# Kernel tuning notes

Measured on AMD Instinct MI355X. Metric: run time of the kernel, lower is better.

## Reference

```python
import jax, jax.numpy as jnp
import numpy as np

N = 50000          # total nodes
B = 10             # graphs in batch
NPG = N // B       # nodes per graph (equal-sized graphs)
E = 800000         # edges
IN_DIM = 128
HID = 128
NHEAD = 4
DHEAD = HID // NHEAD
T = 1000
SLOPE = 0.2        # leaky_relu negative slope
ALPHA_L = 2.0


def _ln(x, g=None, b=None, eps=1e-5):
    mu = jnp.mean(x, axis=-1, keepdims=True)
    var = jnp.var(x, axis=-1, keepdims=True)
    y = (x - mu) * jax.lax.rsqrt(var + eps)
    if g is not None:
        y = y * g + b
    return y


def _gatv2(h, src, dst, Ws, Wd, a, b):
    # DGL GATv2Conv, share_weights=False, residual=False, bias=True, activation=gelu
    fs = (h @ Ws).reshape(N, NHEAD, DHEAD)
    fd = (h @ Wd).reshape(N, NHEAD, DHEAD)
    # per-edge attention logits [E, NHEAD]
    e = jnp.sum(jax.nn.leaky_relu(fs[src] + fd[dst], SLOPE) * a, axis=-1)
    # edge softmax grouped by destination node
    m = jax.ops.segment_max(e, dst, num_segments=N)
    ee = jnp.exp(e - m[dst])
    den = jax.ops.segment_sum(ee, dst, num_segments=N)
    alpha = ee / den[dst]                                  # [E, NHEAD]
    rst = jax.ops.segment_sum(alpha[..., None] * fs[src], dst, num_segments=N)
    rst = jax.nn.gelu(rst + b.reshape(1, NHEAD, DHEAD), approximate=False)
    return rst.reshape(N, HID)


def _forward(x, noise, sab, somab, time_emb,
             Ws0, Wd0, a0, b0, g0, be0,
             Ws1, Wd1, a1, b1, g1, be1,
             Wo1, bo1, Wo2, bo2, src, dst, t):
    # sample_q: statistics-matched signed noise
    miu = jnp.mean(x, axis=0)
    std = jnp.std(x, axis=0, ddof=1)          # torch.std is unbiased
    nz = _ln(noise) * std + miu
    nz = jnp.sign(x) * jnp.abs(nz)
    s1 = jnp.repeat(sab[t], NPG)[:, None]
    s2 = jnp.repeat(somab[t], NPG)[:, None]
    x_t = s1 * x + s2 * nz
    temb = jnp.repeat(time_emb[t], NPG, axis=0)
    # Denoising_Unet
    h = jnp.concatenate([x_t, temb], axis=1)   # [N, IN_DIM+HID]
    h = _ln(_gatv2(h, src, dst, Ws0, Wd0, a0, b0), g0, be0)
    h_in = h
    h = _gatv2(h, src, dst, Ws1, Wd1, a1, b1)
    h = _ln(h + h_in, g1, be1)                 # residual (shapes match)
    out = jax.nn.relu(h @ Wo1 + bo1) @ Wo2 + bo2
    # loss_fn
    mse = jnp.mean((out - x) ** 2)
    on = out / jnp.maximum(jnp.linalg.norm(out, axis=-1, keepdims=True), 1e-12)
    xn = x / jnp.maximum(jnp.linalg.norm(x, axis=-1, keepdims=True), 1e-12)
    cos = jnp.mean((1.0 - jnp.sum(on * xn, axis=-1)) ** ALPHA_L)
    return mse + 0.1 * cos


def setup_inputs() -> dict:
    key = jax.random.key(0)
    ks = jax.random.split(key, 26)
    betas = np.linspace(1e-4, 0.02, T, dtype=np.float64)
    ab = np.cumprod(1.0 - betas)
    s = 0.02
    in0 = IN_DIM + HID
    inp = {}
    inp['x'] = jax.random.normal(ks[0], (N, IN_DIM), jnp.float32)
    inp['noise'] = jax.random.normal(ks[1], (N, IN_DIM), jnp.float32)
    inp['src'] = jax.random.randint(ks[2], (E,), 0, N, dtype=jnp.int32)
    inp['dst'] = jax.random.randint(ks[3], (E,), 0, N, dtype=jnp.int32)
    inp['t'] = jax.random.randint(ks[4], (B,), 0, T, dtype=jnp.int32)
    inp['sab'] = jnp.asarray(np.sqrt(ab), jnp.float32)
    inp['somab'] = jnp.asarray(np.sqrt(1.0 - ab), jnp.float32)
    inp['time_emb'] = jax.random.normal(ks[5], (T, HID), jnp.float32) * s
    inp['Ws0'] = jax.random.normal(ks[6], (in0, HID), jnp.float32) * s
    inp['Wd0'] = jax.random.normal(ks[7], (in0, HID), jnp.float32) * s
    inp['a0'] = jax.random.normal(ks[8], (NHEAD, DHEAD), jnp.float32) * s
    inp['b0'] = jnp.zeros((HID,), jnp.float32)
    inp['g0'] = jnp.ones((HID,), jnp.float32)
    inp['be0'] = jnp.zeros((HID,), jnp.float32)
    inp['Ws1'] = jax.random.normal(ks[9], (HID, HID), jnp.float32) * s
    inp['Wd1'] = jax.random.normal(ks[10], (HID, HID), jnp.float32) * s
    inp['a1'] = jax.random.normal(ks[11], (NHEAD, DHEAD), jnp.float32) * s
    inp['b1'] = jnp.zeros((HID,), jnp.float32)
    inp['g1'] = jnp.ones((HID,), jnp.float32)
    inp['be1'] = jnp.zeros((HID,), jnp.float32)
    inp['Wo1'] = jax.random.normal(ks[12], (HID, HID), jnp.float32) * s
    inp['bo1'] = jnp.zeros((HID,), jnp.float32)
    inp['Wo2'] = jax.random.normal(ks[13], (HID, IN_DIM), jnp.float32) * s
    inp['bo2'] = jnp.zeros((IN_DIM,), jnp.float32)
    return inp


def reference(x, noise, src, dst, t, sab, somab, time_emb,
              Ws0, Wd0, a0, b0, g0, be0,
              Ws1, Wd1, a1, b1, g1, be1,
              Wo1, bo1, Wo2, bo2):
    return _forward(x, noise, sab, somab, time_emb,
                    Ws0, Wd0, a0, b0, g0, be0,
                    Ws1, Wd1, a1, b1, g1, be1,
                    Wo1, bo1, Wo2, bo2, src, dst, t)
```

## Files before the change

kernel.cpp:

```cpp
#include <hip/hip_runtime.h>
#include <hip/hip_bf16.h>
#include <math.h>

#define NN 50000
#define EE 800000
#define NPG 5000

typedef short bf16x8 __attribute__((ext_vector_type(8)));
typedef float f32x4 __attribute__((ext_vector_type(4)));

__device__ __forceinline__ float gelu_exact(float v) {
    return 0.5f * v * (1.0f + erff(v * 0.70710678118654752440f));
}

__device__ __forceinline__ ushort f2b(float f) {
    union { float f; uint u; } v; v.f = f;
    uint r = (v.u + 0x7fffu + ((v.u >> 16) & 1)) >> 16;
    return (ushort)r;
}
__device__ __forceinline__ uint pack2(float a, float b) {
    return (uint)f2b(a) | ((uint)f2b(b) << 16);
}
__device__ __forceinline__ float blo(uint u) {
    union { uint u; float f; } v; v.u = u << 16; return v.f;
}
__device__ __forceinline__ float bhi(uint u) {
    union { uint u; float f; } v; v.u = u & 0xffff0000u; return v.f;
}

__global__ __launch_bounds__(256) void head1_kernel(const float* __restrict__ x,
        float* __restrict__ sums, const int* __restrict__ dst, int* __restrict__ counts,
        const float* __restrict__ Ws0, const float* __restrict__ Wd0,
        const float* __restrict__ Ws1, const float* __restrict__ Wd1,
        const float* __restrict__ Wo1, const float* __restrict__ Wo2,
        ushort* __restrict__ Wt0, ushort* __restrict__ Wt1,
        ushort* __restrict__ Wo1t, ushort* __restrict__ Wo2t) {
    int bid = blockIdx.x;
    int tid = threadIdx.x;
    if (bid < 1024) {
        int col4 = (tid & 31) * 4;
        int rowgrp = tid >> 5;
        float s0 = 0.f, s1 = 0.f, s2 = 0.f, s3 = 0.f;
        float q0 = 0.f, q1 = 0.f, q2 = 0.f, q3 = 0.f;
        for (int r = bid * 8 + rowgrp; r < NN; r += 8192) {
            float4 v = *(const float4*)(x + (size_t)r * 128 + col4);
            s0 += v.x; s1 += v.y; s2 += v.z; s3 += v.w;
            q0 += v.x * v.x; q1 += v.y * v.y; q2 += v.z * v.z; q3 += v.w * v.w;
        }
        s0 += __shfl_xor(s0, 32); s1 += __shfl_xor(s1, 32);
        s2 += __shfl_xor(s2, 32); s3 += __shfl_xor(s3, 32);
        q0 += __shfl_xor(q0, 32); q1 += __shfl_xor(q1, 32);
        q2 += __shfl_xor(q2, 32); q3 += __shfl_xor(q3, 32);
        __shared__ float red[4][32][8];
        int wv = tid >> 6, l = tid & 63;
        if (l < 32) {
            float* p = red[wv][l];
            p[0] = s0; p[1] = s1; p[2] = s2; p[3] = s3;
            p[4] = q0; p[5] = q1; p[6] = q2; p[7] = q3;
        }
        __syncthreads();
        if (tid < 32) {
            float a0 = 0.f, a1 = 0.f, a2 = 0.f, a3 = 0.f;
            float b0 = 0.f, b1 = 0.f, b2 = 0.f, b3 = 0.f;
#pragma unroll
            for (int w = 0; w < 4; ++w) {
                float* p = red[w][tid];
                a0 += p[0]; a1 += p[1]; a2 += p[2]; a3 += p[3];
                b0 += p[4]; b1 += p[5]; b2 += p[6]; b3 += p[7];
            }
            int c = tid * 4;
            atomicAdd(&sums[c], a0); atomicAdd(&sums[c + 1], a1);
            atomicAdd(&sums[c + 2], a2); atomicAdd(&sums[c + 3], a3);
            atomicAdd(&sums[128 + c], b0); atomicAdd(&sums[128 + c + 1], b1);
            atomicAdd(&sums[128 + c + 2], b2); atomicAdd(&sums[128 + c + 3], b3);
        }
    } else if (bid < 4149) {
        int i = (bid - 1024) * 256 + tid;
        if (i < EE) atomicAdd(&counts[dst[i]], 1);
    } else {
        int i = (bid - 4149) * 256 + tid;
        if (i < 65536) {
            int c = i >> 8, k = i & 255;
            const float* W = (c < 128) ? Ws0 : Wd0;
            Wt0[c * 256 + k] = f2b(W[k * 128 + (c & 127)]);
        } else if (i < 98304) {
            int j = i - 65536;
            int c = j >> 7, k = j & 127;
            const float* W = (c < 128) ? Ws1 : Wd1;
            Wt1[c * 128 + k] = f2b(W[k * 128 + (c & 127)]);
        } else if (i < 114688) {
            int j = i - 98304;
            int c = j >> 7, k = j & 127;
            Wo1t[c * 128 + k] = f2b(Wo1[k * 128 + c]);
        } else if (i < 131072) {
            int j = i - 114688;
            int c = j >> 7, k = j & 127;
            Wo2t[c * 128 + k] = f2b(Wo2[k * 128 + c]);
        }
    }
}

__global__ __launch_bounds__(1024) void head2_kernel(const int* __restrict__ counts,
        int* __restrict__ blockSums, float* __restrict__ stats, int n) {
    int bid = blockIdx.x;
    int tid = threadIdx.x;
    if (bid < 49) {
        int i = bid * 1024 + tid;
        int v = (i < n) ? counts[i] : 0;
#pragma unroll
        for (int o = 32; o > 0; o >>= 1) v += __shfl_down(v, o);
        __shared__ int sh[16];
        int lane = tid & 63, wv = tid >> 6;
        if (lane == 0) sh[wv] = v;
        __syncthreads();
        if (tid == 0) {
            int s = 0;
#pragma unroll
            for (int k = 0; k < 16; ++k) s += sh[k];
            blockSums[bid] = s;
        }
    } else {
        if (tid < 128) {
            int c = tid;
            float sum = stats[c], sumsq = stats[128 + c];
            float mu = sum / (float)n;
            float var = (sumsq - sum * sum / (float)n) / (float)(n - 1);
            stats[256 + c] = mu;
            stats[384 + c] = sqrtf(fmaxf(var, 0.f));
        }
    }
}

__global__ __launch_bounds__(1024) void head3_kernel(const float* __restrict__ x,
        const float* __restrict__ noise, const int* __restrict__ t,
        const float* __restrict__ sab, const float* __restrict__ somab,
        const float* __restrict__ temb, const float* __restrict__ stats,
        ushort* __restrict__ h,
        const int* __restrict__ counts, const int* __restrict__ blockSums,
        int* __restrict__ indptr, int* __restrict__ cursor, int n) {
    int bid = blockIdx.x;
    int tid = threadIdx.x;
    if (bid < 3125) {
        int wid = bid * 16 + (tid >> 6);
        int lane = tid & 63;
        int tt = t[wid / NPG];
        float s1 = sab[tt], s2v = somab[tt];
        float2 nz = ((const float2*)noise)[(size_t)wid * 64 + lane];
        float s = nz.x + nz.y;
        float sq = nz.x * nz.x + nz.y * nz.y;
#pragma unroll
        for (int o = 1; o < 64; o <<= 1) { s += __shfl_xor(s, o); sq += __shfl_xor(sq, o); }
        float mu = s * (1.f / 128.f);
        float var = sq * (1.f / 128.f) - mu * mu;
        float r = rsqrtf(var + 1e-5f);
        int f0 = 2 * lane, f1 = f0 + 1;
        float y0 = (nz.x - mu) * r * stats[384 + f0] + stats[256 + f0];
        float y1 = (nz.y - mu) * r * stats[384 + f1] + stats[256 + f1];
        float2 xv = ((const float2*)x)[(size_t)wid * 64 + lane];
        float sg0 = (xv.x > 0.f) ? 1.f : ((xv.x < 0.f) ? -1.f : 0.f);
        float sg1 = (xv.y > 0.f) ? 1.f : ((xv.y < 0.f) ? -1.f : 0.f);
        float n0 = sg0 * fabsf(y0);
        float n1 = sg1 * fabsf(y1);
        float xt0 = s1 * xv.x + s2v * n0;
        float xt1 = s1 * xv.y + s2v * n1;
        uint* row = (uint*)(h + (size_t)wid * 256);
        row[lane] = pack2(xt0, xt1);
        float2 te = ((const float2*)(temb + (size_t)tt * 128))[lane];
        row[64 + lane] = pack2(te.x, te.y);
    } else {
        int b = bid - 3125;
        __shared__ int sOff, sTot;
        if (tid < 64) {
            int v = (tid < 49) ? blockSums[tid] : 0;
            int incl = v;
#pragma unroll
            for (int o = 1; o < 64; o <<= 1) {
                int tv = __shfl_up(incl, o);
                if ((tid & 63) >= o) incl += tv;
            }
            int off = (b == 0) ? 0 : __shfl(incl, b - 1);
            int tot = __shfl(incl, 48);
            if (tid == 0) { sOff = off; sTot = tot; }
        }
        __syncthreads();
        int i = b * 1024 + tid;
        int v = (i < n) ? counts[i] : 0;
        int lane = tid & 63, wv = tid >> 6;
        int incl = v;
#pragma unroll
        for (int o = 1; o < 64; o <<= 1) {
            int tv = __shfl_up(incl, o);
            if (lane >= o) incl += tv;
        }
        __shared__ int wsum[16];
        __shared__ int woff[16];
        if (lane == 63) wsum[wv] = incl;
        __syncthreads();
        if (tid == 0) {
            int s = 0;
#pragma unroll
            for (int k = 0; k < 16; ++k) { woff[k] = s; s += wsum[k]; }
        }
        __syncthreads();
        int ex = incl - v + woff[wv] + sOff;
        if (i < n) { indptr[i] = ex; cursor[i] = ex; }
        if (b == 48 && tid == 0) indptr[n] = sTot;
    }
}

__global__ __launch_bounds__(1024) void scatter_kernel(const int* __restrict__ src,
        const int* __restrict__ dst, int* __restrict__ cursor,
        int* __restrict__ csr_src, int e) {
    int i = blockIdx.x * 1024 + threadIdx.x;
    if (i < e) {
        int p = atomicAdd(&cursor[dst[i]], 1);
        csr_src[p] = src[i];
    }
}

template<int K, int EPI>
__global__ __launch_bounds__(256, 2) void gemm_resW(const ushort* __restrict__ A,
        const ushort* __restrict__ WtA, const ushort* __restrict__ WtB,
        const float* __restrict__ bias,
        ushort* __restrict__ outA, ushort* __restrict__ outB,
        float* __restrict__ Cf, int half, int M) {
    constexpr int K2 = K * 2;
    __shared__ ushort Wl[128 * K];
    int tid = threadIdx.x;
    int wave = tid >> 6, lane = tid & 63;
    int l15 = lane & 15, g = lane >> 4;
    bool isB = blockIdx.x >= half;
    const ushort* Wt = isB ? WtB : WtA;
    ushort* C0 = isB ? outB : outA;
    int mb = isB ? (blockIdx.x - half) : blockIdx.x;

#pragma unroll
    for (int it = 0; it < K / 16; ++it) {
        int q = (it * 256 + tid) * 16;
        int col = q / K2, qk = q % K2;
        int srcb = col * K2 + (qk ^ ((col & 7) << 4));
        *(float4*)((char*)Wl + q) = *(const float4*)((const char*)Wt + srcb);
    }
    __syncthreads();

    int rowBase = mb * 256 + wave * 64;
    f32x4 acc[4][8] = {};

#pragma unroll
    for (int ks = 0; ks < K / 32; ++ks) {
        bf16x8 af[4];
#pragma unroll
        for (int fr = 0; fr < 4; ++fr) {
            int row = rowBase + fr * 16 + l15;
            int rc = min(row, M - 1);
            af[fr] = *(const bf16x8*)(A + (size_t)rc * K + ks * 32 + g * 8);
        }
#pragma unroll
        for (int n = 0; n < 8; ++n) {
            int col = n * 16 + l15;
            int boff = col * K2 + ((ks * 64 + g * 16) ^ ((col & 7) << 4));
            bf16x8 bf = *(const bf16x8*)((const char*)Wl + boff);
#pragma unroll
            for (int fr = 0; fr < 4; ++fr)
                acc[fr][n] = __builtin_amdgcn_mfma_f32_16x16x32_bf16(af[fr], bf, acc[fr][n], 0, 0, 0);
        }
    }

#pragma unroll
    for (int fr = 0; fr < 4; ++fr) {
#pragma unroll
        for (int n = 0; n < 8; ++n) {
            int col = n * 16 + l15;
#pragma unroll
            for (int j = 0; j < 4; ++j) {
                int row = rowBase + fr * 16 + g * 4 + j;
                if (row < M) {
                    float v = acc[fr][n][j];
                    if (EPI == 1) v = fmaxf(v + bias[col], 0.f);
                    if (EPI == 2) v = v + bias[col];
                    if (EPI == 2) Cf[(size_t)row * 128 + col] = v;
                    else          C0[(size_t)row * 128 + col] = f2b(v);
                }
            }
        }
    }
}

__global__ __launch_bounds__(256) void gat_ln_kernel(const ushort* __restrict__ fs,
        const ushort* __restrict__ fd, const float* __restrict__ a,
        const float* __restrict__ bias, const int* __restrict__ indptr,
        const int* __restrict__ csr_src, const float* __restrict__ resid,
        const float* __restrict__ g, const float* __restrict__ be,
        float* __restrict__ outF, ushort* __restrict__ outB, int n) {
    int tid = threadIdx.x;
    int wave = tid >> 6, lane = tid & 63;
    int nodeLocal = wave >> 1;
    int half = wave & 1;
    int wid = blockIdx.x * 2 + nodeLocal;
    int beg = indptr[wid], end = indptr[wid + 1];
    int cnt = end - beg;
    int c0 = (cnt + 1) >> 1;
    int myBeg = beg + (half ? c0 : 0);
    int myCnt = half ? (cnt - c0) : c0;
    const int* ip = csr_src + myBeg;

    uint fdu = ((const uint*)fd)[(size_t)wid * 64 + lane];
    float fd0 = blo(fdu), fd1 = bhi(fdu);
    float a0 = a[2 * lane], a1 = a[2 * lane + 1];
    const uint* fsu = (const uint*)fs;

    int e0 = (0 < myCnt) ? ip[0] : 0;
    int e1 = (1 < myCnt) ? ip[1] : 0;
    int e2 = (2 < myCnt) ? ip[2] : 0;
    int e3 = (3 < myCnt) ? ip[3] : 0;
    int e4 = (4 < myCnt) ? ip[4] : 0;
    int e5 = (5 < myCnt) ? ip[5] : 0;
    int e6 = (6 < myCnt) ? ip[6] : 0;
    int e7 = (7 < myCnt) ? ip[7] : 0;
    uint v0 = fsu[(size_t)e0 * 64 + lane];
    uint v1 = fsu[(size_t)e1 * 64 + lane];
    uint v2 = fsu[(size_t)e2 * 64 + lane];
    uint v3 = fsu[(size_t)e3 * 64 + lane];
    uint v4 = fsu[(size_t)e4 * 64 + lane];
    uint v5 = fsu[(size_t)e5 * 64 + lane];
    uint v6 = fsu[(size_t)e6 * 64 + lane];
    uint v7 = fsu[(size_t)e7 * 64 + lane];

    float den = 0.f, acc0 = 0.f, acc1 = 0.f;
#pragma unroll 4
    for (int j = 0; j < myCnt; ++j) {
        uint cur = v0;
        v0 = v1; v1 = v2; v2 = v3; v3 = v4; v4 = v5; v5 = v6; v6 = v7;
        int nj = j + 8;
        int ni = (nj < myCnt) ? ip[nj] : 0;
        v7 = fsu[(size_t)ni * 64 + lane];
        float c0f = blo(cur), c1f = bhi(cur);
        float t0 = c0f + fd0; t0 = (t0 > 0.f ? t0 : 0.2f * t0) * a0;
        float t1 = c1f + fd1; t1 = (t1 > 0.f ? t1 : 0.2f * t1) * a1;
        float p = t0 + t1;
        p += __shfl_xor(p, 1); p += __shfl_xor(p, 2);
        p += __shfl_xor(p, 4); p += __shfl_xor(p, 8);
        float w = __expf(p);
        den += w;
        acc0 = fmaf(w, c0f, acc0);
        acc1 = fmaf(w, c1f, acc1);
    }

    __shared__ float sAcc[4][64][2];
    __shared__ float sDen[4][64];
    sAcc[wave][lane][0] = acc0;
    sAcc[wave][lane][1] = acc1;
    sDen[wave][lane] = den;
    __syncthreads();
    if (half == 0) {
        acc0 += sAcc[wave + 1][lane][0];
        acc1 += sAcc[wave + 1][lane][1];
        den  += sDen[wave + 1][lane];
        float inv = (cnt > 0) ? 1.f / den : 0.f;
        float r0 = gelu_exact(acc0 * inv + bias[2 * lane]);
        float r1 = gelu_exact(acc1 * inv + bias[2 * lane + 1]);
        if (resid) {
            float2 rr = ((const float2*)resid)[(size_t)wid * 64 + lane];
            r0 += rr.x; r1 += rr.y;
        }
        float s = r0 + r1;
        float sq = r0 * r0 + r1 * r1;
#pragma unroll
        for (int o = 1; o < 64; o <<= 1) { s += __shfl_xor(s, o); sq += __shfl_xor(sq, o); }
        float mu = s * (1.f / 128.f);
        float var = sq * (1.f / 128.f) - mu * mu;
        float rstd = rsqrtf(var + 1e-5f);
        float2 gg = ((const float2*)g)[lane];
        float2 bb = ((const float2*)be)[lane];
        float o0 = (r0 - mu) * rstd * gg.x + bb.x;
        float o1 = (r1 - mu) * rstd * gg.y + bb.y;
        if (outF) ((float2*)outF)[(size_t)wid * 64 + lane] = make_float2(o0, o1);
        if (outB) ((uint*)outB)[(size_t)wid * 64 + lane] = pack2(o0, o1);
    }
}

__global__ __launch_bounds__(256) void loss_partial_kernel(const float* __restrict__ out,
        const float* __restrict__ x, float* __restrict__ partials, int n) {
    __shared__ float sm[8];
    int lane = threadIdx.x & 63;
    int wv = threadIdx.x >> 6;
    int gw = blockIdx.x * 4 + wv;
    float d2 = 0.f, closs = 0.f;
    for (int row = gw; row < n; row += 4096) {
        float2 o = ((const float2*)out)[(size_t)row * 64 + lane];
        float2 xv = ((const float2*)x)[(size_t)row * 64 + lane];
        float e0 = o.x - xv.x, e1 = o.y - xv.y;
        d2 += e0 * e0 + e1 * e1;
        float oo = o.x * o.x + o.y * o.y;
        float xx = xv.x * xv.x + xv.y * xv.y;
        float ox = o.x * xv.x + o.y * xv.y;
#pragma unroll
        for (int s = 1; s < 64; s <<= 1) {
            oo += __shfl_xor(oo, s); xx += __shfl_xor(xx, s); ox += __shfl_xor(ox, s);
        }
        float no = fmaxf(sqrtf(oo), 1e-12f);
        float nx = fmaxf(sqrtf(xx), 1e-12f);
        float cs = 1.f - ox / (no * nx);
        closs += cs * cs;
    }
#pragma unroll
    for (int s = 1; s < 64; s <<= 1) d2 += __shfl_xor(d2, s);
    if (lane == 0) { sm[wv] = d2; sm[4 + wv] = closs; }
    __syncthreads();
    if (threadIdx.x == 0) {
        partials[2 * blockIdx.x] = sm[0] + sm[1] + sm[2] + sm[3];
        partials[2 * blockIdx.x + 1] = sm[4] + sm[5] + sm[6] + sm[7];
    }
}

__global__ __launch_bounds__(1024) void loss_final_kernel(const float* __restrict__ partials,
        float* __restrict__ outp, int nb, int n) {
    __shared__ double sd[32];
    int tid = threadIdx.x;
    double m = 0.0, c = 0.0;
    for (int i = tid; i < nb; i += 1024) { m += partials[2 * i]; c += partials[2 * i + 1]; }
#pragma unroll
    for (int s = 1; s < 64; s <<= 1) { m += __shfl_xor(m, s); c += __shfl_xor(c, s); }
    int wv = tid >> 6, lane = tid & 63;
    if (lane == 0) { sd[wv] = m; sd[16 + wv] = c; }
    __syncthreads();
    if (tid == 0) {
        double mt = 0.0, ct = 0.0;
        for (int i = 0; i < 16; ++i) { mt += sd[i]; ct += sd[16 + i]; }
        outp[0] = (float)(mt / ((double)n * 128.0) + 0.1 * ct / (double)n);
    }
}

extern "C" void kernel_launch(void* const* d_in, const int* in_sizes, int n_in,
                              void* d_out, int out_size, void* d_ws, size_t ws_size,
                              hipStream_t stream) {
    const int N = NN, E = EE;
    const float* x     = (const float*)d_in[0];
    const float* noise = (const float*)d_in[1];
    const int*   src   = (const int*)d_in[2];
    const int*   dst   = (const int*)d_in[3];
    const int*   t     = (const int*)d_in[4];
    const float* sab   = (const float*)d_in[5];
    const float* somab = (const float*)d_in[6];
    const float* temb  = (const float*)d_in[7];
    const float* Ws0   = (const float*)d_in[8];
    const float* Wd0   = (const float*)d_in[9];
    const float* a0    = (const float*)d_in[10];
    const float* b0    = (const float*)d_in[11];
    const float* g0    = (const float*)d_in[12];
    const float* be0   = (const float*)d_in[13];
    const float* Ws1   = (const float*)d_in[14];
    const float* Wd1   = (const float*)d_in[15];
    const float* a1    = (const float*)d_in[16];
    const float* b1    = (const float*)d_in[17];
    const float* g1    = (const float*)d_in[18];
    const float* be1   = (const float*)d_in[19];
    const float* Wo1   = (const float*)d_in[20];
    const float* bo1   = (const float*)d_in[21];
    const float* Wo2   = (const float*)d_in[22];
    const float* bo2   = (const float*)d_in[23];

    float* ws = (float*)d_ws;
    ushort* hB  = (ushort*)ws;
    ushort* Pb  = (ushort*)ws;
    ushort* fsB = (ushort*)(ws + (size_t)N * 128);
    ushort* fdB = (ushort*)(ws + (size_t)N * 192);
    float*  P   = ws + (size_t)N * 256;
    float*  outb = P;
    ushort* Qb  = fdB;
    ushort* z   = fsB;
    float* wtail = ws + (size_t)N * 384;
    ushort* Wt0  = (ushort*)wtail;
    ushort* Wt1  = (ushort*)(wtail + 32768);
    ushort* Wo1t = (ushort*)(wtail + 49152);
    ushort* Wo2t = (ushort*)(wtail + 57344);
    float* stats    = wtail + 65536;
    float* partials = stats + 512;
    int* counts  = (int*)(partials + 2048);
    int* indptr  = counts + N;
    int* cursor  = indptr + N + 1;
    int* csr_src = cursor + N;
    int* blockSums = csr_src + E;

    hipMemsetAsync(stats, 0, 512 * sizeof(float), stream);
    hipMemsetAsync(counts, 0, (size_t)N * sizeof(int), stream);

    head1_kernel<<<4661, 256, 0, stream>>>(x, stats, dst, counts,
                                           Ws0, Wd0, Ws1, Wd1, Wo1, Wo2,
                                           Wt0, Wt1, Wo1t, Wo2t);
    head2_kernel<<<50, 1024, 0, stream>>>(counts, blockSums, stats, N);
    head3_kernel<<<3174, 1024, 0, stream>>>(x, noise, t, sab, somab, temb, stats, hB,
                                            counts, blockSums, indptr, cursor, N);
    scatter_kernel<<<(E + 1023) / 1024, 1024, 0, stream>>>(src, dst, cursor, csr_src, E);

    gemm_resW<256, 0><<<392, 256, 0, stream>>>(hB, Wt0, Wt0 + 128 * 256, nullptr,
                                               fsB, fdB, nullptr, 196, N);
    gat_ln_kernel<<<N / 2, 256, 0, stream>>>(fsB, fdB, a0, b0, indptr, csr_src,
                                             nullptr, g0, be0, P, Pb, N);
    gemm_resW<128, 0><<<392, 256, 0, stream>>>(Pb, Wt1, Wt1 + 128 * 128, nullptr,
                                               fsB, fdB, nullptr, 196, N);
    gat_ln_kernel<<<N / 2, 256, 0, stream>>>(fsB, fdB, a1, b1, indptr, csr_src,
                                             P, g1, be1, nullptr, Qb, N);
    gemm_resW<128, 1><<<196, 256, 0, stream>>>(Qb, Wo1t, Wo1t, bo1,
                                               z, z, nullptr, 196, N);
    gemm_resW<128, 2><<<196, 256, 0, stream>>>(z, Wo2t, Wo2t, bo2,
                                               nullptr, nullptr, outb, 196, N);

    loss_partial_kernel<<<1024, 256, 0, stream>>>(outb, x, partials, N);
    loss_final_kernel<<<1, 1024, 0, stream>>>(partials, (float*)d_out, 1024, N);
}
```

Baseline: 479.2 us.

## Restructure GEMM to K-streamed tiles and use one wave per node in GAT

The GEMM stops keeping the whole weight matrix resident in LDS and instead streams 32-wide K slices of the transposed weights into shared memory. Each block covers 64 rows, and fs/fd are computed together in one 256-column tile instead of two separate block halves. The GAT kernel drops the split of each node's edges across two waves and the shared-memory merge, so one wave now handles one node. This trims LDS use and syncs in GAT and raises the GEMM block count, at the cost of more barriers per K step and less A-fragment reuse in the GEMM, plus longer serial edge loops for high-degree nodes.

```diff
diff --git a/kernel.cpp b/kernel.cpp
--- a/kernel.cpp
+++ b/kernel.cpp
@@ -218,68 +218,64 @@
     }
 }
 
-template<int K, int EPI>
-__global__ __launch_bounds__(256, 2) void gemm_resW(const ushort* __restrict__ A,
-        const ushort* __restrict__ WtA, const ushort* __restrict__ WtB,
-        const float* __restrict__ bias,
-        ushort* __restrict__ outA, ushort* __restrict__ outB,
-        float* __restrict__ Cf, int half, int M) {
-    constexpr int K2 = K * 2;
-    __shared__ ushort Wl[128 * K];
+template<int K, int NCOL, int EPI>
+__global__ __launch_bounds__(256, 2) void mfma_gemm(const ushort* __restrict__ A,
+        const ushort* __restrict__ Wt, const float* __restrict__ bias,
+        ushort* __restrict__ C0, ushort* __restrict__ C1,
+        float* __restrict__ Cf, int M) {
+    constexpr int NFRAG = NCOL / 16;
+    constexpr int KSTEPS = K / 32;
+    __shared__ ushort Bs[32 * NCOL];
     int tid = threadIdx.x;
     int wave = tid >> 6, lane = tid & 63;
     int l15 = lane & 15, g = lane >> 4;
-    bool isB = blockIdx.x >= half;
-    const ushort* Wt = isB ? WtB : WtA;
-    ushort* C0 = isB ? outB : outA;
-    int mb = isB ? (blockIdx.x - half) : blockIdx.x;
-
-#pragma unroll
-    for (int it = 0; it < K / 16; ++it) {
-        int q = (it * 256 + tid) * 16;
-        int col = q / K2, qk = q % K2;
-        int srcb = col * K2 + (qk ^ ((col & 7) << 4));
-        *(float4*)((char*)Wl + q) = *(const float4*)((const char*)Wt + srcb);
-    }
-    __syncthreads();
-
-    int rowBase = mb * 256 + wave * 64;
-    f32x4 acc[4][8] = {};
-
-#pragma unroll
-    for (int ks = 0; ks < K / 32; ++ks) {
-        bf16x8 af[4];
-#pragma unroll
-        for (int fr = 0; fr < 4; ++fr) {
-            int row = rowBase + fr * 16 + l15;
-            int rc = min(row, M - 1);
-            af[fr] = *(const bf16x8*)(A + (size_t)rc * K + ks * 32 + g * 8);
-        }
-#pragma unroll
-        for (int n = 0; n < 8; ++n) {
-            int col = n * 16 + l15;
-            int boff = col * K2 + ((ks * 64 + g * 16) ^ ((col & 7) << 4));
-            bf16x8 bf = *(const bf16x8*)((const char*)Wl + boff);
-#pragma unroll
-            for (int fr = 0; fr < 4; ++fr)
-                acc[fr][n] = __builtin_amdgcn_mfma_f32_16x16x32_bf16(af[fr], bf, acc[fr][n], 0, 0, 0);
-        }
-    }
-
-#pragma unroll
-    for (int fr = 0; fr < 4; ++fr) {
-#pragma unroll
-        for (int n = 0; n < 8; ++n) {
-            int col = n * 16 + l15;
-#pragma unroll
-            for (int j = 0; j < 4; ++j) {
-                int row = rowBase + fr * 16 + g * 4 + j;
-                if (row < M) {
-                    float v = acc[fr][n][j];
-                    if (EPI == 1) v = fmaxf(v + bias[col], 0.f);
-                    if (EPI == 2) v = v + bias[col];
-                    if (EPI == 2) Cf[(size_t)row * 128 + col] = v;
-                    else          C0[(size_t)row * 128 + col] = f2b(v);
+    int rowBase = blockIdx.x * 64 + wave * 16;
+    int r = rowBase + l15;
+    int rc = min(r, M - 1);
+    const ushort* Arow = A + (size_t)rc * K + g * 8;
+
+    f32x4 acc[NFRAG] = {};
+
+    for (int ks = 0; ks < KSTEPS; ++ks) {
+#pragma unroll
+        for (int i = 0; i < NCOL / 64; ++i) {
+            int ch = tid + i * 256;
+            int c = ch >> 2, q = ch & 3;
+            float4 v = *(const float4*)(Wt + (size_t)c * K + ks * 32 + q * 8);
+            int off = c * 64 + ((q * 16) ^ ((c & 7) << 4));
+            *(float4*)((char*)Bs + off) = v;
+        }
+        __syncthreads();
+        bf16x8 af = *(const bf16x8*)(Arow + ks * 32);
+        int roff = l15 * 64 + ((g * 16) ^ ((l15 & 7) << 4));
+#pragma unroll
+        for (int n = 0; n < NFRAG; ++n) {
+            bf16x8 bf = *(const bf16x8*)((const char*)Bs + n * 1024 + roff);
+            acc[n] = __builtin_amdgcn_mfma_f32_16x16x32_bf16(af, bf, acc[n], 0, 0, 0);
+        }
+        __syncthreads();
+    }
+
+#pragma unroll
+    for (int n = 0; n < NFRAG; ++n) {
+        int col = n * 16 + l15;
+#pragma unroll
+        for (int j = 0; j < 4; ++j) {
+            int row = rowBase + g * 4 + j;
+            if (row < M) {
+                float v = acc[n][j];
+                if (EPI == 1) v = fmaxf(v + bias[col], 0.f);
+                if (EPI == 2) v = v + bias[col];
+                if (EPI == 2) {
+                    Cf[(size_t)row * 128 + col] = v;
+                } else {
+                    ushort bv = f2b(v);
+                    if (NCOL == 256) {
+                        if (n < 8) C0[(size_t)row * 128 + col] = bv;
+                        else       C1[(size_t)row * 128 + col - 128] = bv;
+                    } else {
+                        C0[(size_t)row * 128 + col] = bv;
+                    }
                 }
             }
         }
@@ -292,31 +288,24 @@
         const int* __restrict__ csr_src, const float* __restrict__ resid,
         const float* __restrict__ g, const float* __restrict__ be,
         float* __restrict__ outF, ushort* __restrict__ outB, int n) {
-    int tid = threadIdx.x;
-    int wave = tid >> 6, lane = tid & 63;
-    int nodeLocal = wave >> 1;
-    int half = wave & 1;
-    int wid = blockIdx.x * 2 + nodeLocal;
-    int beg = indptr[wid], end = indptr[wid + 1];
-    int cnt = end - beg;
-    int c0 = (cnt + 1) >> 1;
-    int myBeg = beg + (half ? c0 : 0);
-    int myCnt = half ? (cnt - c0) : c0;
-    const int* ip = csr_src + myBeg;
-
+    int wid = (blockIdx.x * blockDim.x + threadIdx.x) >> 6;
+    int lane = threadIdx.x & 63;
+    if (wid >= n) return;
+    int beg = indptr[wid], cnt = indptr[wid + 1] - beg;
+    const int* ip = csr_src + beg;
     uint fdu = ((const uint*)fd)[(size_t)wid * 64 + lane];
     float fd0 = blo(fdu), fd1 = bhi(fdu);
     float a0 = a[2 * lane], a1 = a[2 * lane + 1];
     const uint* fsu = (const uint*)fs;
 
-    int e0 = (0 < myCnt) ? ip[0] : 0;
-    int e1 = (1 < myCnt) ? ip[1] : 0;
-    int e2 = (2 < myCnt) ? ip[2] : 0;
-    int e3 = (3 < myCnt) ? ip[3] : 0;
-    int e4 = (4 < myCnt) ? ip[4] : 0;
-    int e5 = (5 < myCnt) ? ip[5] : 0;
-    int e6 = (6 < myCnt) ? ip[6] : 0;
-    int e7 = (7 < myCnt) ? ip[7] : 0;
+    int e0 = (0 < cnt) ? ip[0] : 0;
+    int e1 = (1 < cnt) ? ip[1] : 0;
+    int e2 = (2 < cnt) ? ip[2] : 0;
+    int e3 = (3 < cnt) ? ip[3] : 0;
+    int e4 = (4 < cnt) ? ip[4] : 0;
+    int e5 = (5 < cnt) ? ip[5] : 0;
+    int e6 = (6 < cnt) ? ip[6] : 0;
+    int e7 = (7 < cnt) ? ip[7] : 0;
     uint v0 = fsu[(size_t)e0 * 64 + lane];
     uint v1 = fsu[(size_t)e1 * 64 + lane];
     uint v2 = fsu[(size_t)e2 * 64 + lane];
@@ -327,12 +316,11 @@
     uint v7 = fsu[(size_t)e7 * 64 + lane];
 
     float den = 0.f, acc0 = 0.f, acc1 = 0.f;
-#pragma unroll 4
-    for (int j = 0; j < myCnt; ++j) {
+    for (int j = 0; j < cnt; ++j) {
         uint cur = v0;
         v0 = v1; v1 = v2; v2 = v3; v3 = v4; v4 = v5; v5 = v6; v6 = v7;
         int nj = j + 8;
-        int ni = (nj < myCnt) ? ip[nj] : 0;
+        int ni = (nj < cnt) ? ip[nj] : 0;
         v7 = fsu[(size_t)ni * 64 + lane];
         float c0f = blo(cur), c1f = bhi(cur);
         float t0 = c0f + fd0; t0 = (t0 > 0.f ? t0 : 0.2f * t0) * a0;
@@ -346,37 +334,26 @@
         acc1 = fmaf(w, c1f, acc1);
     }
 
-    __shared__ float sAcc[4][64][2];
-    __shared__ float sDen[4][64];
-    sAcc[wave][lane][0] = acc0;
-    sAcc[wave][lane][1] = acc1;
-    sDen[wave][lane] = den;
-    __syncthreads();
-    if (half == 0) {
-        acc0 += sAcc[wave + 1][lane][0];
-        acc1 += sAcc[wave + 1][lane][1];
-        den  += sDen[wave + 1][lane];
-        float inv = (cnt > 0) ? 1.f / den : 0.f;
-        float r0 = gelu_exact(acc0 * inv + bias[2 * lane]);
-        float r1 = gelu_exact(acc1 * inv + bias[2 * lane + 1]);
-        if (resid) {
-            float2 rr = ((const float2*)resid)[(size_t)wid * 64 + lane];
-            r0 += rr.x; r1 += rr.y;
-        }
-        float s = r0 + r1;
-        float sq = r0 * r0 + r1 * r1;
-#pragma unroll
-        for (int o = 1; o < 64; o <<= 1) { s += __shfl_xor(s, o); sq += __shfl_xor(sq, o); }
-        float mu = s * (1.f / 128.f);
-        float var = sq * (1.f / 128.f) - mu * mu;
-        float rstd = rsqrtf(var + 1e-5f);
-        float2 gg = ((const float2*)g)[lane];
-        float2 bb = ((const float2*)be)[lane];
-        float o0 = (r0 - mu) * rstd * gg.x + bb.x;
-        float o1 = (r1 - mu) * rstd * gg.y + bb.y;
-        if (outF) ((float2*)outF)[(size_t)wid * 64 + lane] = make_float2(o0, o1);
-        if (outB) ((uint*)outB)[(size_t)wid * 64 + lane] = pack2(o0, o1);
-    }
+    float inv = (cnt > 0) ? 1.f / den : 0.f;
+    float r0 = gelu_exact(acc0 * inv + bias[2 * lane]);
+    float r1 = gelu_exact(acc1 * inv + bias[2 * lane + 1]);
+    if (resid) {
+        float2 rr = ((const float2*)resid)[(size_t)wid * 64 + lane];
+        r0 += rr.x; r1 += rr.y;
+    }
+    float s = r0 + r1;
+    float sq = r0 * r0 + r1 * r1;
+#pragma unroll
+    for (int o = 1; o < 64; o <<= 1) { s += __shfl_xor(s, o); sq += __shfl_xor(sq, o); }
+    float mu = s * (1.f / 128.f);
+    float var = sq * (1.f / 128.f) - mu * mu;
+    float rstd = rsqrtf(var + 1e-5f);
+    float2 gg = ((const float2*)g)[lane];
+    float2 bb = ((const float2*)be)[lane];
+    float o0 = (r0 - mu) * rstd * gg.x + bb.x;
+    float o1 = (r1 - mu) * rstd * gg.y + bb.y;
+    if (outF) ((float2*)outF)[(size_t)wid * 64 + lane] = make_float2(o0, o1);
+    if (outB) ((uint*)outB)[(size_t)wid * 64 + lane] = pack2(o0, o1);
 }
 
 __global__ __launch_bounds__(256) void loss_partial_kernel(const float* __restrict__ out,
@@ -493,18 +470,15 @@
                                             counts, blockSums, indptr, cursor, N);
     scatter_kernel<<<(E + 1023) / 1024, 1024, 0, stream>>>(src, dst, cursor, csr_src, E);
 
-    gemm_resW<256, 0><<<392, 256, 0, stream>>>(hB, Wt0, Wt0 + 128 * 256, nullptr,
-                                               fsB, fdB, nullptr, 196, N);
-    gat_ln_kernel<<<N / 2, 256, 0, stream>>>(fsB, fdB, a0, b0, indptr, csr_src,
-                                             nullptr, g0, be0, P, Pb, N);
-    gemm_resW<128, 0><<<392, 256, 0, stream>>>(Pb, Wt1, Wt1 + 128 * 128, nullptr,
-                                               fsB, fdB, nullptr, 196, N);
-    gat_ln_kernel<<<N / 2, 256, 0, stream>>>(fsB, fdB, a1, b1, indptr, csr_src,
-                                             P, g1, be1, nullptr, Qb, N);
-    gemm_resW<128, 1><<<196, 256, 0, stream>>>(Qb, Wo1t, Wo1t, bo1,
-                                               z, z, nullptr, 196, N);
-    gemm_resW<128, 2><<<196, 256, 0, stream>>>(z, Wo2t, Wo2t, bo2,
-                                               nullptr, nullptr, outb, 196, N);
+    int gemmGrid = (N + 63) / 64;
+    mfma_gemm<256, 256, 0><<<gemmGrid, 256, 0, stream>>>(hB, Wt0, nullptr, fsB, fdB, nullptr, N);
+    gat_ln_kernel<<<(N + 3) / 4, 256, 0, stream>>>(fsB, fdB, a0, b0, indptr, csr_src,
+                                                   nullptr, g0, be0, P, Pb, N);
+    mfma_gemm<128, 256, 0><<<gemmGrid, 256, 0, stream>>>(Pb, Wt1, nullptr, fsB, fdB, nullptr, N);
+    gat_ln_kernel<<<(N + 3) / 4, 256, 0, stream>>>(fsB, fdB, a1, b1, indptr, csr_src,
+                                                   P, g1, be1, nullptr, Qb, N);
+    mfma_gemm<128, 128, 1><<<gemmGrid, 256, 0, stream>>>(Qb, Wo1t, bo1, z, nullptr, nullptr, N);
+    mfma_gemm<128, 128, 2><<<gemmGrid, 256, 0, stream>>>(z, Wo2t, bo2, nullptr, nullptr, outb, N);
 
     loss_partial_kernel<<<1024, 256, 0, stream>>>(outb, x, partials, N);
     loss_final_kernel<<<1, 1024, 0, stream>>>(partials, (float*)d_out, 1024, N);
```

Result: faster. 454.8 us (-5.1%).
